# Optimization experiments

Measured on AMD Instinct MI355X. Metric: run time of the kernel, lower is better.

The kernel has to match this reference:

```python
import jax, jax.numpy as jnp
import numpy as np

N_GAUSS = 3200          # 20*20*8 voxel-center pseudo points
FEAT_DIM = 17
RENDER_H, RENDER_W = 48, 88
GT_H, GT_W = 192, 352
VOXEL_SIZE = 0.8
PC_MIN = np.array([-8.0, -8.0, -3.2], np.float32)
PC_MAX = np.array([8.0, 8.0, 3.2], np.float32)
NUSC_FREQ = np.array([1163161, 2309034, 188743, 2997643, 20317180, 852476, 243808,
                      2457947, 497017, 2731022, 7224789, 214411435, 5565043,
                      63191967, 76098082, 128860031, 141625221, 2307405309], np.float64)


def setup_inputs() -> dict:
    key = jax.random.key(0)
    k1, k2 = jax.random.split(key, 2)
    # pseudo voxel-center grid (get_presudo_xyz): cell centers on a 20x20x8 grid
    gx = (np.arange(20) + 0.5) * VOXEL_SIZE + PC_MIN[0]
    gy = (np.arange(20) + 0.5) * VOXEL_SIZE + PC_MIN[1]
    gz = (np.arange(8) + 0.5) * VOXEL_SIZE + PC_MIN[2]
    X, Y, Z = np.meshgrid(gx, gy, gz, indexing='ij')
    pc_xyz = np.stack([X, Y, Z], -1).reshape(-1, 3).astype(np.float32)
    # distCUDA2 on a regular grid: mean sq dist to 3 NNs == voxel_size^2
    scales = np.full((N_GAUSS, 3), np.log(VOXEL_SIZE), np.float32)  # log(sqrt(v^2))
    rots = np.zeros((N_GAUSS, 4), np.float32); rots[:, 0] = 1.0  # identity quats
    # two cameras looking at the grid (z_cam > 0 for all points)
    vm0 = np.array([[1, 0, 0, 0], [0, -1, 0, 0], [0, 0, -1, 20], [0, 0, 0, 1]], np.float32)
    vm1 = np.array([[0, 1, 0, 0], [0, 0, -1, 0], [-1, 0, 0, 20], [0, 0, 0, 1]], np.float32)
    viewmats = np.stack([vm0, vm1])
    intr = np.array([[100.0, 50.0, RENDER_W / 2.0, RENDER_H / 2.0]] * 2, np.float32)
    cw = (1.0 / np.log(NUSC_FREQ[:17] + 0.001)).astype(np.float32)
    return {
        'voxel_feats': jax.random.normal(k1, (1, N_GAUSS, FEAT_DIM), jnp.float32),
        'opacity': jax.random.uniform(k2, (1, N_GAUSS, 1), jnp.float32),
        'pc_xyz': jnp.asarray(pc_xyz),
        'scales': jnp.asarray(scales),
        'rots': jnp.asarray(rots),
        'viewmats': jnp.asarray(viewmats),
        'intrinsics': jnp.asarray(intr),
        'class_weights': jnp.asarray(cw),
        'gt_sem': jax.random.randint(jax.random.fold_in(key, 1), (2, GT_H, GT_W), 0, 17, jnp.int32),
        'sem_mask': jax.random.randint(jax.random.fold_in(key, 2), (2, GT_H, GT_W), 0, 2, jnp.int32),
    }


def quat_to_rot(q):
    q = q / jnp.linalg.norm(q, axis=-1, keepdims=True)
    w, x, y, z = q[:, 0], q[:, 1], q[:, 2], q[:, 3]
    return jnp.stack([
        jnp.stack([1 - 2 * (y * y + z * z), 2 * (x * y - w * z), 2 * (x * z + w * y)], -1),
        jnp.stack([2 * (x * y + w * z), 1 - 2 * (x * x + z * z), 2 * (y * z - w * x)], -1),
        jnp.stack([2 * (x * z - w * y), 2 * (y * z + w * x), 1 - 2 * (x * x + y * y)], -1),
    ], -2)  # [N,3,3]


def nearest_resize(img, H, W):
    hi, wi = img.shape
    ri = (jnp.arange(H) * hi) // H
    ci = (jnp.arange(W) * wi) // W
    return img[ri][:, ci]


def render_feature_map(feats, opac, xyz, scale, Rq, viewmat, intr):
    fx, fy, cx, cy = intr[0], intr[1], intr[2], intr[3]
    Rw, t = viewmat[:3, :3], viewmat[:3, 3]
    p = xyz @ Rw.T + t                      # [N,3] camera-frame
    z = p[:, 2]
    valid = z > 0.2
    zc = jnp.maximum(z, 0.2)
    u = fx * p[:, 0] / zc + cx
    v = fy * p[:, 1] / zc + cy
    # 3D covariance: Rq diag(s^2) Rq^T, then to camera frame
    cov3d = jnp.einsum('nij,nj,nkj->nik', Rq, scale * scale, Rq)
    cov_c = jnp.einsum('ij,njk,lk->nil', Rw, cov3d, Rw)
    # projection Jacobian (EWA splatting)
    zero = jnp.zeros_like(zc)
    J = jnp.stack([
        jnp.stack([fx / zc, zero, -fx * p[:, 0] / (zc * zc)], -1),
        jnp.stack([zero, fy / zc, -fy * p[:, 1] / (zc * zc)], -1),
    ], -2)                                  # [N,2,3]
    cov2 = jnp.einsum('nij,njk,nlk->nil', J, cov_c, J)
    a = cov2[:, 0, 0] + 0.3
    b = cov2[:, 0, 1]
    c = cov2[:, 1, 1] + 0.3
    det = jnp.maximum(a * c - b * b, 1e-8)
    A, B, C = c / det, -b / det, a / det    # conic
    px = jnp.arange(RENDER_W, dtype=jnp.float32)
    py = jnp.arange(RENDER_H, dtype=jnp.float32)
    dx = px[None, :] - u[:, None]           # [N,W]
    dy = py[None, :] - v[:, None]           # [N,H]
    power = (-0.5 * (A[:, None, None] * dx[:, None, :] ** 2
                     + C[:, None, None] * dy[:, :, None] ** 2)
             - B[:, None, None] * dx[:, None, :] * dy[:, :, None])  # [N,H,W]
    power = jnp.minimum(power, 0.0)
    alpha = jnp.clip(opac[:, None, None] * jnp.exp(power), 0.0, 0.99)
    alpha = alpha * valid[:, None, None].astype(alpha.dtype)
    order = jnp.argsort(z)                  # front-to-back depth sort
    alpha = alpha[order]
    feats_s = feats[order]
    T = jnp.cumprod(1.0 - alpha, axis=0)
    T_excl = jnp.concatenate([jnp.ones_like(T[:1]), T[:-1]], axis=0)
    w = alpha * T_excl                      # composite weights [N,H,W]
    return jnp.einsum('nhw,nc->hwc', w, feats_s)  # [H,W,17]


def masked_weighted_ce(logits, gt, mask, cw):
    logp = jax.nn.log_softmax(logits, -1)
    nll = -jnp.take_along_axis(logp, gt[:, None], axis=1)[:, 0]
    wi = cw[gt] * mask
    return jnp.sum(wi * nll) / jnp.maximum(jnp.sum(wi), 1e-8)


def reference(voxel_feats, opacity, pc_xyz, scales, rots, viewmats, intrinsics,
              class_weights, gt_sem, sem_mask):
    scale = jnp.exp(scales)
    Rq = quat_to_rot(rots)
    B = voxel_feats.shape[0]
    n_cam = viewmats.shape[0]
    loss_batch = 0.0
    for b in range(B):
        feats = voxel_feats[b].reshape(-1, FEAT_DIM)
        opac = opacity[b].reshape(-1)
        loss_cam = 0.0
        for c in range(n_cam):
            img = render_feature_map(feats, opac, pc_xyz, scale, Rq,
                                     viewmats[c], intrinsics[c])
            logits = img.reshape(-1, FEAT_DIM)
            gt = nearest_resize(gt_sem[c], RENDER_H, RENDER_W).reshape(-1)
            m = nearest_resize(sem_mask[c], RENDER_H, RENDER_W).reshape(-1).astype(jnp.float32)
            loss_cam = loss_cam + masked_weighted_ce(logits, gt, m, class_weights)
        loss_batch = loss_batch + loss_cam / n_cam
    return loss_batch / B  # gaussian_sem_weight = 1.0
```

## Files before the change

### kernel.cpp

```cpp
#include <hip/hip_runtime.h>

#define NG 3200
#define NF 17
#define RH 48
#define RW 88
#define NPIX (RH*RW)
#define GTH 192
#define GTW 352
#define NCAM 2
#define CHUNK 200
#define NCHUNK 16

#define Z_OFF    0
#define PU_OFF   (Z_OFF + NCAM*NG)
#define PS_OFF   (PU_OFF + NCAM*NG*6)
#define FS_OFF   (PS_OFF + NCAM*NG*6)
#define PT_OFF   (FS_OFF + NCAM*NG*NF)
#define ACC_OFF  (PT_OFF + NCAM*NCHUNK*18*NPIX)

__global__ __launch_bounds__(256) void k_preproc(
    const float* __restrict__ opac, const float* __restrict__ xyz,
    const float* __restrict__ scales, const float* __restrict__ rots,
    const float* __restrict__ vm, const float* __restrict__ intr,
    float* __restrict__ ws)
{
  int idx = blockIdx.x*blockDim.x + threadIdx.x;
  if (idx >= NCAM*NG) return;
  int cam = idx / NG, g = idx % NG;

  float qw=rots[g*4+0], qx=rots[g*4+1], qy=rots[g*4+2], qz=rots[g*4+3];
  float qn = rsqrtf(qw*qw+qx*qx+qy*qy+qz*qz);
  qw*=qn; qx*=qn; qy*=qn; qz*=qn;
  float R[3][3];
  R[0][0]=1.f-2.f*(qy*qy+qz*qz); R[0][1]=2.f*(qx*qy-qw*qz); R[0][2]=2.f*(qx*qz+qw*qy);
  R[1][0]=2.f*(qx*qy+qw*qz); R[1][1]=1.f-2.f*(qx*qx+qz*qz); R[1][2]=2.f*(qy*qz-qw*qx);
  R[2][0]=2.f*(qx*qz-qw*qy); R[2][1]=2.f*(qy*qz+qw*qx); R[2][2]=1.f-2.f*(qx*qx+qy*qy);

  float s2[3];
  #pragma unroll
  for (int k=0;k<3;k++){ float s=expf(scales[g*3+k]); s2[k]=s*s; }

  float M[3][3];
  #pragma unroll
  for(int i=0;i<3;i++)
    #pragma unroll
    for(int j=0;j<3;j++)
      M[i][j] = R[i][0]*s2[0]*R[j][0] + R[i][1]*s2[1]*R[j][1] + R[i][2]*s2[2]*R[j][2];

  const float* Vm = vm + cam*16;
  float Rw[3][3], t[3];
  #pragma unroll
  for(int i=0;i<3;i++){
    #pragma unroll
    for(int j=0;j<3;j++) Rw[i][j]=Vm[i*4+j];
    t[i]=Vm[i*4+3];
  }

  float T1[3][3];
  #pragma unroll
  for(int i=0;i<3;i++)
    #pragma unroll
    for(int j=0;j<3;j++)
      T1[i][j] = Rw[i][0]*M[0][j] + Rw[i][1]*M[1][j] + Rw[i][2]*M[2][j];
  float V[3][3];
  #pragma unroll
  for(int i=0;i<3;i++)
    #pragma unroll
    for(int j=0;j<3;j++)
      V[i][j] = T1[i][0]*Rw[j][0] + T1[i][1]*Rw[j][1] + T1[i][2]*Rw[j][2];

  float X=xyz[g*3+0], Y=xyz[g*3+1], Zp=xyz[g*3+2];
  float p0 = Rw[0][0]*X + Rw[0][1]*Y + Rw[0][2]*Zp + t[0];
  float p1 = Rw[1][0]*X + Rw[1][1]*Y + Rw[1][2]*Zp + t[1];
  float p2 = Rw[2][0]*X + Rw[2][1]*Y + Rw[2][2]*Zp + t[2];

  float z  = p2;
  float zc = fmaxf(z, 0.2f);
  float fx=intr[cam*4+0], fy=intr[cam*4+1], cx=intr[cam*4+2], cy=intr[cam*4+3];
  float u = fx*p0/zc + cx;
  float v = fy*p1/zc + cy;

  float j00 = fx/zc, j02 = -fx*p0/(zc*zc);
  float j11 = fy/zc, j12 = -fy*p1/(zc*zc);
  float c00 = j00*j00*V[0][0] + 2.f*j00*j02*V[0][2] + j02*j02*V[2][2];
  float c01 = j00*(V[0][1]*j11 + V[0][2]*j12) + j02*(V[2][1]*j11 + V[2][2]*j12);
  float c11 = j11*j11*V[1][1] + 2.f*j11*j12*V[1][2] + j12*j12*V[2][2];

  float a = c00 + 0.3f, b = c01, c = c11 + 0.3f;
  float det = fmaxf(a*c - b*b, 1e-8f);
  float A = c/det, Bc = -b/det, C = a/det;
  float opv = (z > 0.2f) ? opac[g] : 0.0f;

  ws[Z_OFF + idx] = z;
  float* P = ws + PU_OFF + (size_t)idx*6;
  P[0]=u; P[1]=v; P[2]=A; P[3]=Bc; P[4]=C; P[5]=opv;
}

__global__ __launch_bounds__(256) void k_sort(
    const float* __restrict__ feats, float* __restrict__ ws)
{
  __shared__ float zsh[NG];
  int cam = blockIdx.y;
  for (int i=threadIdx.x; i<NG; i+=256) zsh[i] = ws[Z_OFF + cam*NG + i];
  __syncthreads();

  int wave = threadIdx.x >> 6, lane = threadIdx.x & 63;
  int g = blockIdx.x*4 + wave;
  float zi = zsh[g];
  int rank = 0;
  #pragma unroll 5
  for (int k=0; k<NG/64; k++){
    int j = k*64 + lane;
    float zj = zsh[j];
    rank += ((zj < zi) || (zj == zi && j < g)) ? 1 : 0;
  }
  #pragma unroll
  for (int off=32; off>0; off>>=1) rank += __shfl_down(rank, off, 64);
  rank = __shfl(rank, 0, 64);

  const float* src = ws + PU_OFF + (size_t)(cam*NG+g)*6;
  if (lane < 6) (ws + PS_OFF + (size_t)(cam*NG+rank)*6)[lane] = src[lane];
  if (lane < NF) (ws + FS_OFF + (size_t)(cam*NG+rank)*NF)[lane] = feats[g*NF+lane];
}

__global__ __launch_bounds__(256) void k_render(float* __restrict__ ws)
{
  __shared__ float sp[CHUNK*6];
  __shared__ float sf[CHUNK*NF];
  int cam = blockIdx.z, chunk = blockIdx.y;
  int g0 = chunk*CHUNK;
  const float* psrc = ws + PS_OFF + (size_t)(cam*NG+g0)*6;
  for (int i=threadIdx.x; i<CHUNK*6; i+=256) sp[i]=psrc[i];
  const float* fsrc = ws + FS_OFF + (size_t)(cam*NG+g0)*NF;
  for (int i=threadIdx.x; i<CHUNK*NF; i+=256) sf[i]=fsrc[i];
  __syncthreads();

  int pix = blockIdx.x*256 + threadIdx.x;
  if (pix >= NPIX) return;
  float px = (float)(pix % RW), py = (float)(pix / RW);

  float T = 1.0f;
  float F[NF];
  #pragma unroll
  for(int k=0;k<NF;k++) F[k]=0.f;

  for (int g=0; g<CHUNK; g++){
    const float* P = sp + g*6;
    float dx = px - P[0], dy = py - P[1];
    float power = -0.5f*(P[2]*dx*dx + P[4]*dy*dy) - P[3]*dx*dy;
    power = fminf(power, 0.f);
    float alpha = fminf(P[5]*__expf(power), 0.99f);
    float w = alpha*T;
    T *= (1.f - alpha);
    const float* f = sf + g*NF;
    #pragma unroll
    for(int k=0;k<NF;k++) F[k] += w*f[k];
  }

  float* out = ws + PT_OFF + (size_t)((cam*NCHUNK+chunk)*18)*NPIX + pix;
  #pragma unroll
  for(int k=0;k<NF;k++) out[k*NPIX]=F[k];
  out[17*NPIX]=T;
}

__global__ __launch_bounds__(256) void k_loss(
    const int* __restrict__ gt, const int* __restrict__ mask,
    const float* __restrict__ cw, float* __restrict__ ws)
{
  int cam = blockIdx.y;
  int pix = blockIdx.x*256 + threadIdx.x;
  float num = 0.f, den = 0.f;
  if (pix < NPIX) {
    float img[NF];
    #pragma unroll
    for(int k=0;k<NF;k++) img[k]=0.f;
    float Trun = 1.f;
    for (int c=0; c<NCHUNK; c++){
      const float* base = ws + PT_OFF + (size_t)((cam*NCHUNK+c)*18)*NPIX + pix;
      #pragma unroll
      for(int k=0;k<NF;k++) img[k] += Trun*base[k*NPIX];
      Trun *= base[17*NPIX];
    }
    int row = pix / RW, col = pix % RW;
    int gofs = cam*GTH*GTW + (row*4)*GTW + col*4;
    int gi = gt[gofs];
    float mi = (float)mask[gofs];
    float mx = img[0];
    #pragma unroll
    for(int k=1;k<NF;k++) mx = fmaxf(mx, img[k]);
    float s = 0.f;
    #pragma unroll
    for(int k=0;k<NF;k++) s += expf(img[k]-mx);
    float lse = mx + logf(s);
    float nll = lse - img[gi];
    float wi  = cw[gi]*mi;
    num = wi*nll; den = wi;
  }
  #pragma unroll
  for (int off=32; off>0; off>>=1){
    num += __shfl_down(num, off, 64);
    den += __shfl_down(den, off, 64);
  }
  if ((threadIdx.x & 63) == 0){
    atomicAdd(ws + ACC_OFF + cam*2 + 0, num);
    atomicAdd(ws + ACC_OFF + cam*2 + 1, den);
  }
}

__global__ void k_final(const float* __restrict__ ws, float* __restrict__ out)
{
  float l0 = ws[ACC_OFF+0]/fmaxf(ws[ACC_OFF+1], 1e-8f);
  float l1 = ws[ACC_OFF+2]/fmaxf(ws[ACC_OFF+3], 1e-8f);
  out[0] = 0.5f*(l0 + l1);
}

extern "C" void kernel_launch(void* const* d_in, const int* in_sizes, int n_in,
                              void* d_out, int out_size, void* d_ws, size_t ws_size,
                              hipStream_t stream) {
  const float* vf   = (const float*)d_in[0];
  const float* op   = (const float*)d_in[1];
  const float* xyz  = (const float*)d_in[2];
  const float* sc   = (const float*)d_in[3];
  const float* rt   = (const float*)d_in[4];
  const float* vm   = (const float*)d_in[5];
  const float* intr = (const float*)d_in[6];
  const float* cw   = (const float*)d_in[7];
  const int*   gt   = (const int*)d_in[8];
  const int*   mask = (const int*)d_in[9];
  float* ws  = (float*)d_ws;
  float* out = (float*)d_out;

  hipMemsetAsync(ws + ACC_OFF, 0, 4*sizeof(float), stream);
  k_preproc<<<dim3((NCAM*NG+255)/256), 256, 0, stream>>>(op, xyz, sc, rt, vm, intr, ws);
  k_sort   <<<dim3(NG/4, NCAM), 256, 0, stream>>>(vf, ws);
  k_render <<<dim3((NPIX+255)/256, NCHUNK, NCAM), 256, 0, stream>>>(ws);
  k_loss   <<<dim3((NPIX+255)/256, NCAM), 256, 0, stream>>>(gt, mask, cw, ws);
  k_final  <<<1,1,0,stream>>>(ws, out);
}
```

Measured before the change: 153.4 us.

## Split render into smaller chunks, packed-FMA features, add hierarchical partial combine

New measurement: 152.9 us. No clear change (-0.3%).

```diff
diff --git a/kernel.cpp b/kernel.cpp
--- a/kernel.cpp
+++ b/kernel.cpp
@@ -2,21 +2,27 @@
 
 #define NG 3200
 #define NF 17
+#define NFP 18
 #define RH 48
 #define RW 88
 #define NPIX (RH*RW)
 #define GTH 192
 #define GTW 352
 #define NCAM 2
-#define CHUNK 200
-#define NCHUNK 16
+#define CHUNK 64
+#define NCHUNK 50
+#define GPC 5
+#define NGROUP 10
+
+typedef float v2f __attribute__((ext_vector_type(2)));
 
 #define Z_OFF    0
 #define PU_OFF   (Z_OFF + NCAM*NG)
 #define PS_OFF   (PU_OFF + NCAM*NG*6)
 #define FS_OFF   (PS_OFF + NCAM*NG*6)
-#define PT_OFF   (FS_OFF + NCAM*NG*NF)
-#define ACC_OFF  (PT_OFF + NCAM*NCHUNK*18*NPIX)
+#define PT_OFF   (FS_OFF + NCAM*NG*NFP)
+#define GP_OFF   (PT_OFF + NCAM*NCHUNK*18*NPIX)
+#define ACC_OFF  (GP_OFF + NCAM*NGROUP*18*NPIX)
 
 __global__ __launch_bounds__(256) void k_preproc(
     const float* __restrict__ opac, const float* __restrict__ xyz,
@@ -120,19 +126,21 @@
 
   const float* src = ws + PU_OFF + (size_t)(cam*NG+g)*6;
   if (lane < 6) (ws + PS_OFF + (size_t)(cam*NG+rank)*6)[lane] = src[lane];
-  if (lane < NF) (ws + FS_OFF + (size_t)(cam*NG+rank)*NF)[lane] = feats[g*NF+lane];
+  if (lane < NFP) (ws + FS_OFF + (size_t)(cam*NG+rank)*NFP)[lane] =
+                     (lane < NF) ? feats[g*NF+lane] : 0.0f;
 }
 
 __global__ __launch_bounds__(256) void k_render(float* __restrict__ ws)
 {
   __shared__ float sp[CHUNK*6];
-  __shared__ float sf[CHUNK*NF];
+  __shared__ v2f   sf2[CHUNK*(NFP/2)];
   int cam = blockIdx.z, chunk = blockIdx.y;
   int g0 = chunk*CHUNK;
   const float* psrc = ws + PS_OFF + (size_t)(cam*NG+g0)*6;
   for (int i=threadIdx.x; i<CHUNK*6; i+=256) sp[i]=psrc[i];
-  const float* fsrc = ws + FS_OFF + (size_t)(cam*NG+g0)*NF;
-  for (int i=threadIdx.x; i<CHUNK*NF; i+=256) sf[i]=fsrc[i];
+  const float* fsrc = ws + FS_OFF + (size_t)(cam*NG+g0)*NFP;
+  float* sff = (float*)sf2;
+  for (int i=threadIdx.x; i<CHUNK*NFP; i+=256) sff[i]=fsrc[i];
   __syncthreads();
 
   int pix = blockIdx.x*256 + threadIdx.x;
@@ -140,10 +148,11 @@
   float px = (float)(pix % RW), py = (float)(pix / RW);
 
   float T = 1.0f;
-  float F[NF];
-  #pragma unroll
-  for(int k=0;k<NF;k++) F[k]=0.f;
-
+  v2f F2[9];
+  #pragma unroll
+  for(int k=0;k<9;k++) F2[k]=(v2f)(0.f);
+
+  #pragma unroll 4
   for (int g=0; g<CHUNK; g++){
     const float* P = sp + g*6;
     float dx = px - P[0], dy = py - P[1];
@@ -152,12 +161,35 @@
     float alpha = fminf(P[5]*__expf(power), 0.99f);
     float w = alpha*T;
     T *= (1.f - alpha);
-    const float* f = sf + g*NF;
-    #pragma unroll
-    for(int k=0;k<NF;k++) F[k] += w*f[k];
+    v2f w2; w2.x = w; w2.y = w;
+    const v2f* f2 = sf2 + g*(NFP/2);
+    #pragma unroll
+    for(int k=0;k<9;k++) F2[k] += w2*f2[k];
   }
 
   float* out = ws + PT_OFF + (size_t)((cam*NCHUNK+chunk)*18)*NPIX + pix;
+  const float* Ff = (const float*)F2;
+  #pragma unroll
+  for(int k=0;k<NF;k++) out[k*NPIX]=Ff[k];
+  out[17*NPIX]=T;
+}
+
+__global__ __launch_bounds__(256) void k_combine(float* __restrict__ ws)
+{
+  int cam = blockIdx.z, grp = blockIdx.y;
+  int pix = blockIdx.x*256 + threadIdx.x;
+  if (pix >= NPIX) return;
+  float F[NF];
+  #pragma unroll
+  for(int k=0;k<NF;k++) F[k]=0.f;
+  float T = 1.f;
+  for (int c=grp*GPC; c<grp*GPC+GPC; c++){
+    const float* base = ws + PT_OFF + (size_t)((cam*NCHUNK+c)*18)*NPIX + pix;
+    #pragma unroll
+    for(int k=0;k<NF;k++) F[k] += T*base[k*NPIX];
+    T *= base[17*NPIX];
+  }
+  float* out = ws + GP_OFF + (size_t)((cam*NGROUP+grp)*18)*NPIX + pix;
   #pragma unroll
   for(int k=0;k<NF;k++) out[k*NPIX]=F[k];
   out[17*NPIX]=T;
@@ -175,8 +207,8 @@
     #pragma unroll
     for(int k=0;k<NF;k++) img[k]=0.f;
     float Trun = 1.f;
-    for (int c=0; c<NCHUNK; c++){
-      const float* base = ws + PT_OFF + (size_t)((cam*NCHUNK+c)*18)*NPIX + pix;
+    for (int c=0; c<NGROUP; c++){
+      const float* base = ws + GP_OFF + (size_t)((cam*NGROUP+c)*18)*NPIX + pix;
       #pragma unroll
       for(int k=0;k<NF;k++) img[k] += Trun*base[k*NPIX];
       Trun *= base[17*NPIX];
@@ -234,6 +266,7 @@
   k_preproc<<<dim3((NCAM*NG+255)/256), 256, 0, stream>>>(op, xyz, sc, rt, vm, intr, ws);
   k_sort   <<<dim3(NG/4, NCAM), 256, 0, stream>>>(vf, ws);
   k_render <<<dim3((NPIX+255)/256, NCHUNK, NCAM), 256, 0, stream>>>(ws);
+  k_combine<<<dim3((NPIX+255)/256, NGROUP, NCAM), 256, 0, stream>>>(ws);
   k_loss   <<<dim3((NPIX+255)/256, NCAM), 256, 0, stream>>>(gt, mask, cw, ws);
   k_final  <<<1,1,0,stream>>>(ws, out);
 }
```
